# Performance work log

Measured on AMD Instinct MI355X. Metric: run time of the kernel, lower is better.

Reference implementation:

```python
import jax, jax.numpy as jnp
import numpy as np

EPS = 1e-5
NUM_CLASSES = 35
STYLE_LEN = 128


def conv3x3(x, w, b):
    # x: [B,C,H,W], w: [O,I,3,3] (OIHW), SAME padding, stride 1
    y = jax.lax.conv_general_dilated(x, w, (1, 1), 'SAME',
                                     dimension_numbers=('NCHW', 'OIHW', 'NCHW'))
    return y + b[None, :, None, None]


def instance_norm(x):
    # InstanceNorm2d(affine=False): per-sample, per-channel over H,W; biased var
    mu = jnp.mean(x, axis=(2, 3), keepdims=True)
    var = jnp.mean((x - mu) ** 2, axis=(2, 3), keepdims=True)
    return (x - mu) * jax.lax.rsqrt(var + EPS)


def setup_inputs() -> dict:
    key = jax.random.key(0)
    ks = jax.random.split(key, 20)
    B, C, H, W = 4, 256, 128, 256
    J, S = NUM_CLASSES, STYLE_LEN
    s = 0.05
    inp = {
        'x': jax.random.normal(ks[0], (B, C, H, W), jnp.float32),
        'seg_labels': jax.random.randint(ks[1], (B, H, W), 0, J),
        'style_codes': jax.random.normal(ks[2], (B, J, S), jnp.float32),
        # per-class FC: fc_w[j] is [out,in] like torch Linear
        'fc_w': jax.random.normal(ks[3], (J, S, S), jnp.float32) * s,
        'fc_b': jax.random.normal(ks[4], (J, S), jnp.float32) * s,
        'conv_gamma_w': jax.random.normal(ks[5], (C, S, 3, 3), jnp.float32) * s,
        'conv_gamma_b': jax.random.normal(ks[6], (C,), jnp.float32) * s,
        'conv_beta_w': jax.random.normal(ks[7], (C, S, 3, 3), jnp.float32) * s,
        'conv_beta_b': jax.random.normal(ks[8], (C,), jnp.float32) * s,
        # SPADE (sean=True): mlp_shared conv label_nc->128, then gamma/beta 128->C
        'mlp_w': jax.random.normal(ks[9], (128, J, 3, 3), jnp.float32) * s,
        'mlp_b': jax.random.normal(ks[10], (128,), jnp.float32) * s,
        'sp_gamma_w': jax.random.normal(ks[11], (C, 128, 3, 3), jnp.float32) * s,
        'sp_gamma_b': jax.random.normal(ks[12], (C,), jnp.float32) * s,
        'sp_beta_w': jax.random.normal(ks[13], (C, 128, 3, 3), jnp.float32) * s,
        'sp_beta_b': jax.random.normal(ks[14], (C,), jnp.float32) * s,
        'blending_gamma': jnp.zeros((1,), jnp.float32),
        'blending_beta': jnp.zeros((1,), jnp.float32),
    }
    return inp


def reference(x, seg_labels, style_codes, fc_w, fc_b,
              conv_gamma_w, conv_gamma_b, conv_beta_w, conv_beta_b,
              mlp_w, mlp_b, sp_gamma_w, sp_gamma_b, sp_beta_w, sp_beta_b,
              blending_gamma, blending_beta):
    # one-hot segmap [B,J,H,W]; same resolution as x so nearest interp is identity
    segmap = jax.nn.one_hot(seg_labels, NUM_CLASSES, axis=1, dtype=x.dtype)

    normalized = instance_norm(x)

    # per-class style FC: mu[b,j,:] = relu(fc_w[j] @ style_codes[b,j] + fc_b[j])
    mu = jax.nn.relu(jnp.einsum('bjd,jod->bjo', style_codes, fc_w) + fc_b[None])
    # gather-compute-scatter: each pixel receives the style vector of its class
    middle_avg = jnp.einsum('bjhw,bjc->bchw', segmap, mu)  # [B,128,H,W]

    gamma_avg = conv3x3(middle_avg, conv_gamma_w, conv_gamma_b)
    beta_avg = conv3x3(middle_avg, conv_beta_w, conv_beta_b)

    # SPADE branch (sean): gamma/beta from segmap
    actv = jax.nn.relu(conv3x3(segmap, mlp_w, mlp_b))
    gamma_spade = conv3x3(actv, sp_gamma_w, sp_gamma_b)
    beta_spade = conv3x3(actv, sp_beta_w, sp_beta_b)

    ga = jax.nn.sigmoid(blending_gamma)[0]
    ba = jax.nn.sigmoid(blending_beta)[0]
    gamma_final = ga * gamma_avg + (1 - ga) * gamma_spade
    beta_final = ba * beta_avg + (1 - ba) * beta_spade
    return normalized * (1 + gamma_final) + beta_final
```

## Files before the change

kernel.cpp:

```cpp
#include <hip/hip_runtime.h>
#include <stdint.h>

typedef __attribute__((ext_vector_type(8))) short short8;
typedef __attribute__((ext_vector_type(4))) float f32x4;

#define HP 130
#define WPAD 258
#define CIN 256

#define AS1 __attribute__((address_space(1)))
#define AS3 __attribute__((address_space(3)))

__device__ __forceinline__ unsigned short f2bf(float f) {
  unsigned int x = __float_as_uint(f);
  x = x + 0x7fffu + ((x >> 16) & 1u);
  return (unsigned short)(x >> 16);
}

__global__ __launch_bounds__(256) void k_pre(
    const float* __restrict__ sty, const float* __restrict__ fcw,
    const float* __restrict__ fcb, float* __restrict__ mu,
    const float* __restrict__ mlpw, float* __restrict__ mlpT,
    const float* __restrict__ cgb, const float* __restrict__ cbb,
    const float* __restrict__ sgb, const float* __restrict__ sbb,
    const float* __restrict__ blg, const float* __restrict__ blb,
    float* __restrict__ bias)
{
  int bid = blockIdx.x, tid = threadIdx.x;
  if (bid < 140) {
    int b = bid / 35, j = bid - 35 * b;
    __shared__ float ss[128];
    if (tid < 128) ss[tid] = sty[((size_t)b * 35 + j) * 128 + tid];
    __syncthreads();
    if (tid < 128) {
      int o = tid;
      const float4* wr = (const float4*)(fcw + ((size_t)j * 128 + o) * 128);
      const float4* sv = (const float4*)ss;
      float acc = fcb[j * 128 + o];
      #pragma unroll 8
      for (int d = 0; d < 32; ++d) {
        float4 wv = wr[d], s4 = sv[d];
        acc += wv.x * s4.x + wv.y * s4.y + wv.z * s4.z + wv.w * s4.w;
      }
      mu[((size_t)b * 35 + j) * 128 + o] = fmaxf(acc, 0.f);
    }
  } else {
    int t = (bid - 140) * 256 + tid;
    if (t < 40320) {
      int o = t & 127;
      int jt = t >> 7;
      mlpT[(size_t)jt * 128 + o] = mlpw[((size_t)o * 35 + (jt / 9)) * 9 + (jt % 9)];
    }
    if (t < 256) {
      float ga = 1.f / (1.f + expf(-blg[0]));
      float ba = 1.f / (1.f + expf(-blb[0]));
      bias[t]       = ga * cgb[t] + (1.f - ga) * sgb[t];
      bias[256 + t] = ba * cbb[t] + (1.f - ba) * sbb[t];
    }
  }
}

__global__ __launch_bounds__(256) void k_mid(
    const float* __restrict__ x, float* __restrict__ stats,
    const int* __restrict__ seg, const float* __restrict__ mu,
    const float* __restrict__ mlpT, const float* __restrict__ mlpb,
    unsigned short* __restrict__ U,
    const float* __restrict__ cgw, const float* __restrict__ cbw,
    const float* __restrict__ sgw, const float* __restrict__ sbw,
    const float* __restrict__ blg, const float* __restrict__ blb,
    unsigned short* __restrict__ Wp)
{
  int bid = blockIdx.x, t = threadIdx.x;
  if (bid < 1024) {
    int bc = bid;
    const float* p = x + (size_t)bc * 32768;
    float s = 0.f, s2 = 0.f;
    #pragma unroll 4
    for (int i = 0; i < 32; ++i) {
      float4 v = *(const float4*)(p + (size_t)i * 1024 + t * 4);
      s  += v.x + v.y + v.z + v.w;
      s2 += v.x * v.x + v.y * v.y + v.z * v.z + v.w * v.w;
    }
    #pragma unroll
    for (int off2 = 32; off2 > 0; off2 >>= 1) {
      s  += __shfl_down(s, off2);
      s2 += __shfl_down(s2, off2);
    }
    __shared__ float red[8];
    int lane = t & 63, wv = t >> 6;
    if (lane == 0) { red[wv] = s; red[4 + wv] = s2; }
    __syncthreads();
    if (t == 0) {
      float S  = red[0] + red[1] + red[2] + red[3];
      float S2 = red[4] + red[5] + red[6] + red[7];
      float mean = S * (1.f / 32768.f);
      float var  = S2 * (1.f / 32768.f) - mean * mean;
      stats[bc] = mean;
      stats[1024 + bc] = rsqrtf(var + 1e-5f);
    }
  } else if (bid < 17408) {
    int blk = bid - 1024;
    int b = blk >> 12, rem = blk & 4095;
    int h = rem >> 5, w0 = (rem & 31) << 3;
    int p = t >> 5, q = t & 31;
    int w = w0 + p;
    unsigned short* up = U + (((size_t)(b * HP + h + 1)) * WPAD + (w + 1)) * CIN;
    union { uint4 v4; unsigned short s[8]; } u;
    if (q < 16) {
      int lab = seg[((size_t)b * 128 + h) * 256 + w];
      const float4* mrow = (const float4*)(mu + ((size_t)(b * 35 + lab)) * 128 + q * 8);
      float4 v0 = mrow[0], v1 = mrow[1];
      u.s[0] = f2bf(v0.x); u.s[1] = f2bf(v0.y); u.s[2] = f2bf(v0.z); u.s[3] = f2bf(v0.w);
      u.s[4] = f2bf(v1.x); u.s[5] = f2bf(v1.y); u.s[6] = f2bf(v1.z); u.s[7] = f2bf(v1.w);
      *(uint4*)(up + q * 8) = u.v4;
    } else {
      int o0 = (q - 16) * 8;
      float a[8];
      #pragma unroll
      for (int j = 0; j < 8; ++j) a[j] = mlpb[o0 + j];
      #pragma unroll
      for (int kh = 0; kh < 3; ++kh) {
        int hh = h + kh - 1;
        if ((unsigned)hh < 128u) {
          #pragma unroll
          for (int kw = 0; kw < 3; ++kw) {
            int ww = w + kw - 1;
            if ((unsigned)ww < 256u) {
              int lab2 = seg[((size_t)b * 128 + hh) * 256 + ww];
              const float4* wr = (const float4*)(mlpT + ((size_t)lab2 * 9 + kh * 3 + kw) * 128 + o0);
              float4 v0 = wr[0], v1 = wr[1];
              a[0] += v0.x; a[1] += v0.y; a[2] += v0.z; a[3] += v0.w;
              a[4] += v1.x; a[5] += v1.y; a[6] += v1.z; a[7] += v1.w;
            }
          }
        }
      }
      #pragma unroll
      for (int j = 0; j < 8; ++j) u.s[j] = f2bf(fmaxf(a[j], 0.f));
      *(uint4*)(up + 128 + o0) = u.v4;
    }
  } else if (bid < 17795) {
    int tt = (bid - 17408) * 256 + t;
    if (tt >= 98816) return;
    int sub = tt & 31, pi = tt >> 5;
    int b = pi / 772, r = pi - b * 772;
    int h, w;
    if (r < 258)      { h = 0;   w = r; }
    else if (r < 516) { h = 129; w = r - 258; }
    else if (r < 644) { h = r - 516 + 1; w = 0; }
    else              { h = r - 644 + 1; w = 257; }
    ((uint4*)U)[((size_t)(b * HP + h) * WPAD + w) * 32 + sub] = (uint4){0, 0, 0, 0};
  } else {
    int gid = (bid - 17795) * 256 + t;
    int lane = gid & 63;
    int cc = (gid >> 6) & 7;
    int rest = gid >> 9;
    int tap = rest % 9;
    int vf = rest / 9;
    int v = vf * 16 + (lane & 15);
    int c = v >> 1, g = v & 1;
    int ci0 = cc * 32 + (lane >> 4) * 8;
    float ga = 1.f / (1.f + expf(-blg[0]));
    float ba = 1.f / (1.f + expf(-blb[0]));
    float sc = g ? ba : ga;
    const float* wavg = g ? cbw : cgw;
    const float* wsp  = g ? sbw : sgw;
    union { uint4 v4; unsigned short s[8]; } u;
    #pragma unroll
    for (int jj = 0; jj < 8; ++jj) {
      int ci = ci0 + jj;
      float val;
      if (ci < 128) val = sc * wavg[((size_t)c * 128 + ci) * 9 + tap];
      else          val = (1.f - sc) * wsp[((size_t)c * 128 + (ci - 128)) * 9 + tap];
      u.s[jj] = f2bf(val);
    }
    int vfgrp = vf >> 2, mfi = vf & 3;
    uint4* dst = (uint4*)Wp + ((size_t)(((vfgrp * 8 + cc) * 9 + tap) * 4 + mfi)) * 64 + lane;
    *dst = u.v4;
  }
}


#define WAITV_(vm, lg) asm volatile("s_waitcnt vmcnt(" #vm ") lgkmcnt(" #lg ")" ::: "memory")
#define WAITV(vm, lg) do { WAITV_(vm, lg); __builtin_amdgcn_sched_barrier(0); } while (0)
#define WAITL(lg) do { asm volatile("s_waitcnt lgkmcnt(" #lg ")" ::: "memory"); __builtin_amdgcn_sched_barrier(0); } while (0)

#define MM(AS, BS, H) do {                                                     \
    __builtin_amdgcn_s_setprio(1);                                             \
    _Pragma("unroll")                                                          \
    for (int mf_ = 0; mf_ < 4; ++mf_)                                          \
      _Pragma("unroll")                                                        \
      for (int nf_ = 0; nf_ < 4; ++nf_)                                        \
        acc[mf_][(H) * 4 + nf_] = __builtin_amdgcn_mfma_f32_16x16x32_bf16(     \
            afr##AS[mf_], bfr##BS[nf_], acc[mf_][(H) * 4 + nf_], 0, 0, 0);     \
    __builtin_amdgcn_s_setprio(0);                                             \
  } while (0)

#define LOADA(NS) do {                                                         \
    aptr += 4096;                                                              \
    afr##NS[0] = *(const short8*)(aptr);                                       \
    afr##NS[1] = *(const short8*)(aptr + 1024);                                \
    afr##NS[2] = *(const short8*)(aptr + 2048);                                \
    afr##NS[3] = *(const short8*)(aptr + 3072);                                \
  } while (0)

#define LOADB(NS, T, H) do {                                                   \
    bfr##NS[0] = *(const short8*)(lbuf + off[T] + (H) * 4096);                 \
    bfr##NS[1] = *(const short8*)(lbuf + off[T] + (H) * 4096 + 1024);          \
    bfr##NS[2] = *(const short8*)(lbuf + off[T] + (H) * 4096 + 2048);          \
    bfr##NS[3] = *(const short8*)(lbuf + off[T] + (H) * 4096 + 3072);          \
  } while (0)

#define STG(SI) do {                                                           \
    __builtin_amdgcn_global_load_lds((const AS1 unsigned int*)gsrc[SI],        \
        (AS3 unsigned int*)((SI) < 6 ? (stbw + (SI) * 4096) : (stb + 24576)),  \
        16, 0, 0);                                                             \
    gsrc[SI] += 64;                                                            \
  } while (0)

__global__ __launch_bounds__(256, 2) void k_conv(
    const float* __restrict__ x, const uint4* __restrict__ U,
    const char* __restrict__ Wp, const float* __restrict__ bias,
    const float* __restrict__ stats, float* __restrict__ out)
{
  int bid = blockIdx.x;
  int xcd = bid & 7, i0 = bid >> 3;
  int pt = xcd * 128 + (i0 >> 1);
  int mt = i0 & 1;
  int b = pt >> 8, rem = pt & 255;
  int h0 = rem >> 1, w0 = (rem & 1) << 7;
  int tid = threadIdx.x;
  int lane = tid & 63, wid = tid >> 6;
  int lo = lane & 15, hi = lane >> 4;

  __shared__ uint4 Ubuf[2][1600];

  const char* gsrc[7];
  #pragma unroll
  for (int i = 0; i < 7; ++i) {
    int row = (i < 6) ? (wid + 4 * i) : 24;
    int slot = row * 64 + lane;
    int P = slot >> 2, sp = slot & 3;
    int sl = sp ^ ((P >> 1) & 3);
    int r = P / 130, pix = P - r * 130;
    gsrc[i] = (const char*)U +
        (size_t)(((b * HP + h0 + r) * WPAD + (w0 + pix)) * CIN + sl * 8) * 2;
  }

  f32x4 acc[4][8];
  #pragma unroll
  for (int i = 0; i < 4; ++i)
    #pragma unroll
    for (int j = 0; j < 8; ++j) acc[i][j] = (f32x4){0.f, 0.f, 0.f, 0.f};

  int vfgrp = mt * 4 + wid;
  const char* aptr = Wp + (size_t)vfgrp * 294912 + lane * 16;

  int off[9];
  #pragma unroll
  for (int t = 0; t < 9; ++t) {
    int Pb = (t / 3) * 130 + (t % 3) + lo;
    off[t] = Pb * 64 + ((hi ^ ((Pb >> 1) & 3)) << 4);
  }

  const char* lbuf = (const char*)&Ubuf[0][0];
  char* stb = (char*)&Ubuf[1][0];

  {
    char* stb0 = (char*)&Ubuf[0][0];
    char* stbw0 = stb0 + wid * 1024;
    #pragma unroll
    for (int i = 0; i < 7; ++i) {
      __builtin_amdgcn_global_load_lds((const AS1 unsigned int*)gsrc[i],
          (AS3 unsigned int*)(i < 6 ? (stbw0 + i * 4096) : (stb0 + 24576)), 16, 0, 0);
      gsrc[i] += 64;
    }
  }
  short8 afr0[4], afr1[4], bfr0[4], bfr1[4];
  afr0[0] = *(const short8*)(aptr);
  afr0[1] = *(const short8*)(aptr + 1024);
  afr0[2] = *(const short8*)(aptr + 2048);
  afr0[3] = *(const short8*)(aptr + 3072);
  WAITV(4, 0);
  __builtin_amdgcn_s_barrier();

  #pragma unroll 1
  for (int cc = 0; cc < 7; ++cc) {
    char* stbw = stb + wid * 1024;
    LOADB(0, 0, 0);
    LOADA(1); STG(0); LOADB(1, 0, 1); WAITV(5, 4); MM(0, 0, 0);
              LOADB(0, 1, 0);        WAITL(4);     MM(0, 1, 1);
    LOADA(0); STG(1); LOADB(1, 1, 1); WAITV(6, 4); MM(1, 0, 0);
              LOADB(0, 2, 0);        WAITL(4);     MM(1, 1, 1);
    LOADA(1); STG(2); LOADB(1, 2, 1); WAITV(6, 4); MM(0, 0, 0);
              LOADB(0, 3, 0);        WAITL(4);     MM(0, 1, 1);
    LOADA(0); STG(3); LOADB(1, 3, 1); WAITV(6, 4); MM(1, 0, 0);
              LOADB(0, 4, 0);        WAITL(4);     MM(1, 1, 1);
    LOADA(1); STG(4); LOADB(1, 4, 1); WAITV(6, 4); MM(0, 0, 0);
              LOADB(0, 5, 0);        WAITL(4);     MM(0, 1, 1);
    LOADA(0); STG(5); LOADB(1, 5, 1); WAITV(6, 4); MM(1, 0, 0);
              LOADB(0, 6, 0);        WAITL(4);     MM(1, 1, 1);
    LOADA(1); STG(6); LOADB(1, 6, 1); WAITV(6, 4); MM(0, 0, 0);
              LOADB(0, 7, 0);        WAITL(4);     MM(0, 1, 1);
    LOADA(0);         LOADB(1, 7, 1); WAITV(5, 4); MM(1, 0, 0);
              LOADB(0, 8, 0);        WAITL(4);     MM(1, 1, 1);
    LOADA(1);         LOADB(1, 8, 1); WAITV(4, 4); MM(0, 0, 0);
                                     WAITV(4, 0);  MM(0, 1, 1);
    __builtin_amdgcn_s_barrier();
    { const char* tmp = lbuf; lbuf = (const char*)stb; stb = (char*)tmp; }
    { short8 t0 = afr1[0]; afr0[0] = t0; t0 = afr1[1]; afr0[1] = t0;
      t0 = afr1[2]; afr0[2] = t0; t0 = afr1[3]; afr0[3] = t0; }
  }
  {
    LOADB(0, 0, 0);
    LOADA(1); LOADB(1, 0, 1); WAITV(4, 4); MM(0, 0, 0);
              LOADB(0, 1, 0); WAITL(4);    MM(0, 1, 1);
    LOADA(0); LOADB(1, 1, 1); WAITV(4, 4); MM(1, 0, 0);
              LOADB(0, 2, 0); WAITL(4);    MM(1, 1, 1);
    LOADA(1); LOADB(1, 2, 1); WAITV(4, 4); MM(0, 0, 0);
              LOADB(0, 3, 0); WAITL(4);    MM(0, 1, 1);
    LOADA(0); LOADB(1, 3, 1); WAITV(4, 4); MM(1, 0, 0);
              LOADB(0, 4, 0); WAITL(4);    MM(1, 1, 1);
    LOADA(1); LOADB(1, 4, 1); WAITV(4, 4); MM(0, 0, 0);
              LOADB(0, 5, 0); WAITL(4);    MM(0, 1, 1);
    LOADA(0); LOADB(1, 5, 1); WAITV(4, 4); MM(1, 0, 0);
              LOADB(0, 6, 0); WAITL(4);    MM(1, 1, 1);
    LOADA(1); LOADB(1, 6, 1); WAITV(4, 4); MM(0, 0, 0);
              LOADB(0, 7, 0); WAITL(4);    MM(0, 1, 1);
    LOADA(0); LOADB(1, 7, 1); WAITV(4, 4); MM(1, 0, 0);
              LOADB(0, 8, 0); WAITL(4);    MM(1, 1, 1);
              LOADB(1, 8, 1); WAITV(0, 4); MM(0, 0, 0);
                              WAITL(0);    MM(0, 1, 1);
  }

  #pragma unroll
  for (int mf = 0; mf < 4; ++mf) {
    int vbase = mt * 256 + wid * 64 + mf * 16 + hi * 4;
    #pragma unroll
    for (int p = 0; p < 2; ++p) {
      int c = (vbase >> 1) + p;
      float bg = bias[c], bb = bias[256 + c];
      float mean = stats[b * 256 + c], rs = stats[1024 + b * 256 + c];
      const float* xrow = x + ((size_t)(b * 256 + c) * 128 + h0) * 256 + w0;
      float* orow = out + ((size_t)(b * 256 + c) * 128 + h0) * 256 + w0;
      #pragma unroll
      for (int nf = 0; nf < 8; ++nf) {
        int pix = nf * 16 + lo;
        float g  = acc[mf][nf][2 * p]     + bg;
        float bt = acc[mf][nf][2 * p + 1] + bb;
        float xv = xrow[pix];
        orow[pix] = (xv - mean) * rs * (1.f + g) + bt;
      }
    }
  }
}

extern "C" void kernel_launch(void* const* d_in, const int* in_sizes, int n_in,
                              void* d_out, int out_size, void* d_ws, size_t ws_size,
                              hipStream_t stream)
{
  const float* x    = (const float*)d_in[0];
  const int*   seg  = (const int*)d_in[1];
  const float* sty  = (const float*)d_in[2];
  const float* fcw  = (const float*)d_in[3];
  const float* fcb  = (const float*)d_in[4];
  const float* cgw  = (const float*)d_in[5];
  const float* cgb  = (const float*)d_in[6];
  const float* cbw  = (const float*)d_in[7];
  const float* cbb  = (const float*)d_in[8];
  const float* mlpw = (const float*)d_in[9];
  const float* mlpb = (const float*)d_in[10];
  const float* sgw  = (const float*)d_in[11];
  const float* sgb  = (const float*)d_in[12];
  const float* sbw  = (const float*)d_in[13];
  const float* sbb  = (const float*)d_in[14];
  const float* blg  = (const float*)d_in[15];
  const float* blb  = (const float*)d_in[16];
  float* out = (float*)d_out;

  char* ws = (char*)d_ws;
  const size_t U_BYTES = (size_t)4 * HP * WPAD * CIN * 2;
  size_t off = 0;
  unsigned short* U = (unsigned short*)(ws + off); off += U_BYTES + 262144;
  char* Wp   = ws + off;           off += (size_t)512 * 256 * 9 * 2;
  float* mu  = (float*)(ws + off); off += (size_t)4 * 35 * 128 * 4;
  float* mlpT= (float*)(ws + off); off += (size_t)35 * 9 * 128 * 4;
  float* bias= (float*)(ws + off); off += 2048;
  float* stats=(float*)(ws + off); off += 8192;
  if (ws_size < off) return;

  k_pre <<<dim3(298),   dim3(256), 0, stream>>>(
      sty, fcw, fcb, mu, mlpw, mlpT, cgb, cbb, sgb, sbb, blg, blb, bias);
  k_mid <<<dim3(18371), dim3(256), 0, stream>>>(
      x, stats, seg, mu, mlpT, mlpb, U, cgw, cbw, sgw, sbw, blg, blb,
      (unsigned short*)Wp);
  k_conv<<<dim3(2048),  dim3(256), 0, stream>>>(
      x, (const uint4*)U, Wp, bias, stats, out);
}
```

Before: 324.9 us.

## Halve per-wave output tile in conv and change LDS staging layout for higher occupancy

Each wave now computes 2 MFMA row-fragments instead of 4, so the output-channel dimension is split across 4 blocks per pixel tile and the grid doubles to 4096 blocks. Launch bounds rise to 3 blocks per CU, and the weight packing moves to pairs of fragments. The LDS staging layout changes from a per-pixel XOR-swizzled layout to a slice-major layout with a fixed base offset per lane, which removes the per-tap offset table. The aim is to lower register pressure to raise occupancy and hide latency better. The cost is that each staged input tile is loaded and reused by twice as many blocks, which doubles global and LDS traffic per FLOP, and the new layout may cause LDS bank conflicts.

```diff
diff --git a/kernel.cpp b/kernel.cpp
--- a/kernel.cpp
+++ b/kernel.cpp
@@ -174,8 +174,8 @@
       else          val = (1.f - sc) * wsp[((size_t)c * 128 + (ci - 128)) * 9 + tap];
       u.s[jj] = f2bf(val);
     }
-    int vfgrp = vf >> 2, mfi = vf & 3;
-    uint4* dst = (uint4*)Wp + ((size_t)(((vfgrp * 8 + cc) * 9 + tap) * 4 + mfi)) * 64 + lane;
+    int vfpair = vf >> 1, mfi = vf & 1;
+    uint4* dst = (uint4*)Wp + ((size_t)(((vfpair * 8 + cc) * 9 + tap) * 2 + mfi)) * 64 + lane;
     *dst = u.v4;
   }
 }
@@ -188,7 +188,7 @@
 #define MM(AS, BS, H) do {                                                     \
     __builtin_amdgcn_s_setprio(1);                                             \
     _Pragma("unroll")                                                          \
-    for (int mf_ = 0; mf_ < 4; ++mf_)                                          \
+    for (int mf_ = 0; mf_ < 2; ++mf_)                                          \
       _Pragma("unroll")                                                        \
       for (int nf_ = 0; nf_ < 4; ++nf_)                                        \
         acc[mf_][(H) * 4 + nf_] = __builtin_amdgcn_mfma_f32_16x16x32_bf16(     \
@@ -197,18 +197,17 @@
   } while (0)
 
 #define LOADA(NS) do {                                                         \
-    aptr += 4096;                                                              \
+    aptr += 2048;                                                              \
     afr##NS[0] = *(const short8*)(aptr);                                       \
     afr##NS[1] = *(const short8*)(aptr + 1024);                                \
-    afr##NS[2] = *(const short8*)(aptr + 2048);                                \
-    afr##NS[3] = *(const short8*)(aptr + 3072);                                \
   } while (0)
 
+#define BOFF(T, H) (((T) / 3) * 8320 + ((T) % 3) * 16 + (H) * 1024)
 #define LOADB(NS, T, H) do {                                                   \
-    bfr##NS[0] = *(const short8*)(lbuf + off[T] + (H) * 4096);                 \
-    bfr##NS[1] = *(const short8*)(lbuf + off[T] + (H) * 4096 + 1024);          \
-    bfr##NS[2] = *(const short8*)(lbuf + off[T] + (H) * 4096 + 2048);          \
-    bfr##NS[3] = *(const short8*)(lbuf + off[T] + (H) * 4096 + 3072);          \
+    bfr##NS[0] = *(const short8*)(lbuf + pbase + BOFF(T, H));                  \
+    bfr##NS[1] = *(const short8*)(lbuf + pbase + BOFF(T, H) + 256);            \
+    bfr##NS[2] = *(const short8*)(lbuf + pbase + BOFF(T, H) + 512);            \
+    bfr##NS[3] = *(const short8*)(lbuf + pbase + BOFF(T, H) + 768);            \
   } while (0)
 
 #define STG(SI) do {                                                           \
@@ -218,15 +217,15 @@
     gsrc[SI] += 64;                                                            \
   } while (0)
 
-__global__ __launch_bounds__(256, 2) void k_conv(
+__global__ __launch_bounds__(256, 3) void k_conv(
     const float* __restrict__ x, const uint4* __restrict__ U,
     const char* __restrict__ Wp, const float* __restrict__ bias,
     const float* __restrict__ stats, float* __restrict__ out)
 {
   int bid = blockIdx.x;
   int xcd = bid & 7, i0 = bid >> 3;
-  int pt = xcd * 128 + (i0 >> 1);
-  int mt = i0 & 1;
+  int pt = xcd * 128 + (i0 >> 2);
+  int mt = i0 & 3;
   int b = pt >> 8, rem = pt & 255;
   int h0 = rem >> 1, w0 = (rem & 1) << 7;
   int tid = threadIdx.x;
@@ -239,29 +238,23 @@
   #pragma unroll
   for (int i = 0; i < 7; ++i) {
     int row = (i < 6) ? (wid + 4 * i) : 24;
-    int slot = row * 64 + lane;
-    int P = slot >> 2, sp = slot & 3;
-    int sl = sp ^ ((P >> 1) & 3);
-    int r = P / 130, pix = P - r * 130;
+    int L = row * 64 + lane;
+    int rsl = L / 130, px = L - rsl * 130;
+    int r = rsl >> 2, sl = rsl & 3;
     gsrc[i] = (const char*)U +
-        (size_t)(((b * HP + h0 + r) * WPAD + (w0 + pix)) * CIN + sl * 8) * 2;
-  }
-
-  f32x4 acc[4][8];
+        (size_t)(((b * HP + h0 + r) * WPAD + (w0 + px)) * CIN + sl * 8) * 2;
+  }
+
+  f32x4 acc[2][8];
   #pragma unroll
-  for (int i = 0; i < 4; ++i)
+  for (int i = 0; i < 2; ++i)
     #pragma unroll
     for (int j = 0; j < 8; ++j) acc[i][j] = (f32x4){0.f, 0.f, 0.f, 0.f};
 
-  int vfgrp = mt * 4 + wid;
-  const char* aptr = Wp + (size_t)vfgrp * 294912 + lane * 16;
-
-  int off[9];
-  #pragma unroll
-  for (int t = 0; t < 9; ++t) {
-    int Pb = (t / 3) * 130 + (t % 3) + lo;
-    off[t] = Pb * 64 + ((hi ^ ((Pb >> 1) & 3)) << 4);
-  }
+  int vfpair = mt * 4 + wid;
+  const char* aptr = Wp + (size_t)vfpair * 147456 + lane * 16;
+
+  int pbase = hi * 2080 + lo * 16;
 
   const char* lbuf = (const char*)&Ubuf[0][0];
   char* stb = (char*)&Ubuf[1][0];
@@ -276,66 +269,63 @@
       gsrc[i] += 64;
     }
   }
-  short8 afr0[4], afr1[4], bfr0[4], bfr1[4];
+  short8 afr0[2], afr1[2], bfr0[4], bfr1[4];
   afr0[0] = *(const short8*)(aptr);
   afr0[1] = *(const short8*)(aptr + 1024);
-  afr0[2] = *(const short8*)(aptr + 2048);
-  afr0[3] = *(const short8*)(aptr + 3072);
-  WAITV(4, 0);
+  WAITV(2, 0);
   __builtin_amdgcn_s_barrier();
 
   #pragma unroll 1
   for (int cc = 0; cc < 7; ++cc) {
     char* stbw = stb + wid * 1024;
     LOADB(0, 0, 0);
-    LOADA(1); STG(0); LOADB(1, 0, 1); WAITV(5, 4); MM(0, 0, 0);
+    LOADA(1); STG(0); LOADB(1, 0, 1); WAITV(3, 4); MM(0, 0, 0);
               LOADB(0, 1, 0);        WAITL(4);     MM(0, 1, 1);
-    LOADA(0); STG(1); LOADB(1, 1, 1); WAITV(6, 4); MM(1, 0, 0);
+    LOADA(0); STG(1); LOADB(1, 1, 1); WAITV(4, 4); MM(1, 0, 0);
               LOADB(0, 2, 0);        WAITL(4);     MM(1, 1, 1);
-    LOADA(1); STG(2); LOADB(1, 2, 1); WAITV(6, 4); MM(0, 0, 0);
+    LOADA(1); STG(2); LOADB(1, 2, 1); WAITV(4, 4); MM(0, 0, 0);
               LOADB(0, 3, 0);        WAITL(4);     MM(0, 1, 1);
-    LOADA(0); STG(3); LOADB(1, 3, 1); WAITV(6, 4); MM(1, 0, 0);
+    LOADA(0); STG(3); LOADB(1, 3, 1); WAITV(4, 4); MM(1, 0, 0);
               LOADB(0, 4, 0);        WAITL(4);     MM(1, 1, 1);
-    LOADA(1); STG(4); LOADB(1, 4, 1); WAITV(6, 4); MM(0, 0, 0);
+    LOADA(1); STG(4); LOADB(1, 4, 1); WAITV(4, 4); MM(0, 0, 0);
               LOADB(0, 5, 0);        WAITL(4);     MM(0, 1, 1);
-    LOADA(0); STG(5); LOADB(1, 5, 1); WAITV(6, 4); MM(1, 0, 0);
+    LOADA(0); STG(5); LOADB(1, 5, 1); WAITV(4, 4); MM(1, 0, 0);
               LOADB(0, 6, 0);        WAITL(4);     MM(1, 1, 1);
-    LOADA(1); STG(6); LOADB(1, 6, 1); WAITV(6, 4); MM(0, 0, 0);
+    LOADA(1); STG(6); LOADB(1, 6, 1); WAITV(4, 4); MM(0, 0, 0);
               LOADB(0, 7, 0);        WAITL(4);     MM(0, 1, 1);
-    LOADA(0);         LOADB(1, 7, 1); WAITV(5, 4); MM(1, 0, 0);
+    LOADA(0);         LOADB(1, 7, 1); WAITV(3, 4); MM(1, 0, 0);
               LOADB(0, 8, 0);        WAITL(4);     MM(1, 1, 1);
-    LOADA(1);         LOADB(1, 8, 1); WAITV(4, 4); MM(0, 0, 0);
-                                     WAITV(4, 0);  MM(0, 1, 1);
+    LOADA(1);         LOADB(1, 8, 1); WAITV(2, 4); MM(0, 0, 0);
+                                     WAITV(2, 0);  MM(0, 1, 1);
     __builtin_amdgcn_s_barrier();
     { const char* tmp = lbuf; lbuf = (const char*)stb; stb = (char*)tmp; }
-    { short8 t0 = afr1[0]; afr0[0] = t0; t0 = afr1[1]; afr0[1] = t0;
-      t0 = afr1[2]; afr0[2] = t0; t0 = afr1[3]; afr0[3] = t0; }
+    { short8 t0 = afr1[0]; afr0[0] = t0; t0 = afr1[1]; afr0[1] = t0; }
   }
   {
     LOADB(0, 0, 0);
-    LOADA(1); LOADB(1, 0, 1); WAITV(4, 4); MM(0, 0, 0);
+    LOADA(1); LOADB(1, 0, 1); WAITV(2, 4); MM(0, 0, 0);
               LOADB(0, 1, 0); WAITL(4);    MM(0, 1, 1);
-    LOADA(0); LOADB(1, 1, 1); WAITV(4, 4); MM(1, 0, 0);
+    LOADA(0); LOADB(1, 1, 1); WAITV(2, 4); MM(1, 0, 0);
               LOADB(0, 2, 0); WAITL(4);    MM(1, 1, 1);
-    LOADA(1); LOADB(1, 2, 1); WAITV(4, 4); MM(0, 0, 0);
+    LOADA(1); LOADB(1, 2, 1); WAITV(2, 4); MM(0, 0, 0);
               LOADB(0, 3, 0); WAITL(4);    MM(0, 1, 1);
-    LOADA(0); LOADB(1, 3, 1); WAITV(4, 4); MM(1, 0, 0);
+    LOADA(0); LOADB(1, 3, 1); WAITV(2, 4); MM(1, 0, 0);
               LOADB(0, 4, 0); WAITL(4);    MM(1, 1, 1);
-    LOADA(1); LOADB(1, 4, 1); WAITV(4, 4); MM(0, 0, 0);
+    LOADA(1); LOADB(1, 4, 1); WAITV(2, 4); MM(0, 0, 0);
               LOADB(0, 5, 0); WAITL(4);    MM(0, 1, 1);
-    LOADA(0); LOADB(1, 5, 1); WAITV(4, 4); MM(1, 0, 0);
+    LOADA(0); LOADB(1, 5, 1); WAITV(2, 4); MM(1, 0, 0);
               LOADB(0, 6, 0); WAITL(4);    MM(1, 1, 1);
-    LOADA(1); LOADB(1, 6, 1); WAITV(4, 4); MM(0, 0, 0);
+    LOADA(1); LOADB(1, 6, 1); WAITV(2, 4); MM(0, 0, 0);
               LOADB(0, 7, 0); WAITL(4);    MM(0, 1, 1);
-    LOADA(0); LOADB(1, 7, 1); WAITV(4, 4); MM(1, 0, 0);
+    LOADA(0); LOADB(1, 7, 1); WAITV(2, 4); MM(1, 0, 0);
               LOADB(0, 8, 0); WAITL(4);    MM(1, 1, 1);
               LOADB(1, 8, 1); WAITV(0, 4); MM(0, 0, 0);
                               WAITL(0);    MM(0, 1, 1);
   }
 
   #pragma unroll
-  for (int mf = 0; mf < 4; ++mf) {
-    int vbase = mt * 256 + wid * 64 + mf * 16 + hi * 4;
+  for (int mf = 0; mf < 2; ++mf) {
+    int vbase = vfpair * 32 + mf * 16 + hi * 4;
     #pragma unroll
     for (int p = 0; p < 2; ++p) {
       int c = (vbase >> 1) + p;
@@ -394,6 +384,6 @@
   k_mid <<<dim3(18371), dim3(256), 0, stream>>>(
       x, stats, seg, mu, mlpT, mlpb, U, cgw, cbw, sgw, sbw, blg, blb,
       (unsigned short*)Wp);
-  k_conv<<<dim3(2048),  dim3(256), 0, stream>>>(
+  k_conv<<<dim3(4096),  dim3(256), 0, stream>>>(
       x, (const uint4*)U, Wp, bias, stats, out);
 }
```

Measured after the change: 382.9 us. 17.9% more time.
